# Kernel optimization log

Measured on AMD Instinct MI355X. Metric: run time of the kernel, lower is better.

Reference implementation:

```python
import jax, jax.numpy as jnp
import numpy as np

SIGMAS = (15, 40, 80)  # multi-scale Retinex scales; kernel_size = 2*sigma+1


def _gauss1d(ksize, sigma):
    # kornia.filters.get_gaussian_kernel1d: centered, normalized gaussian
    x = jnp.arange(ksize, dtype=jnp.float32) - (ksize - 1) / 2.0
    g = jnp.exp(-(x * x) / (2.0 * sigma * sigma))
    return g / g.sum()


def _gaussian_blur(img, sigma):
    # img: [B,C,H,W]; kornia gaussian_blur2d: separable depthwise conv,
    # reflect padding, kernel_size = 2*sigma+1
    ksize = int(2 * sigma + 1)
    pad = ksize // 2
    C = img.shape[1]
    k = _gauss1d(ksize, float(sigma))
    xp = jnp.pad(img, ((0, 0), (0, 0), (pad, pad), (pad, pad)), mode='reflect')
    kh = jnp.broadcast_to(k.reshape(1, 1, ksize, 1), (C, 1, ksize, 1))
    kw = jnp.broadcast_to(k.reshape(1, 1, 1, ksize), (C, 1, 1, ksize))
    dn = ('NCHW', 'OIHW', 'NCHW')
    y = jax.lax.conv_general_dilated(xp, kh, (1, 1), 'VALID',
                                     dimension_numbers=dn, feature_group_count=C)
    y = jax.lax.conv_general_dilated(y, kw, (1, 1), 'VALID',
                                     dimension_numbers=dn, feature_group_count=C)
    return y


def setup_inputs() -> dict:
    key = jax.random.key(0)
    B, C, H, W = 8, 3, 1024, 1024
    img = jax.random.uniform(key, (B, C, H, W), dtype=jnp.float32)  # positive, log-safe
    sigmas = jnp.broadcast_to(jnp.array(SIGMAS, dtype=jnp.int32), (B, len(SIGMAS)))
    return {"img": img, "sigmas": sigmas}


def reference(img, sigmas):
    # sigmas determine kernel sizes -> must be static (concrete) values.
    # All batch rows share the same sigma set, so the per-batch loop of the
    # original collapses into batched whole-tensor blurs (identical math).
    sig = np.asarray(sigmas)
    S = sig.shape[1]
    x = img.astype(jnp.float32) + 1e-6
    log_x = jnp.log(x)
    acc = jnp.zeros_like(x)
    for j in range(S):  # small fixed loop over scales (S=3)
        ill = _gaussian_blur(x, int(sig[0, j])) + 1e-6
        acc = acc + (log_x - jnp.log(ill))
    retinex = acc / S
    rmin = retinex.min()
    rmax = retinex.max()
    return (retinex - rmin) / (rmax - rmin) * 255.0
```

## Files before the change

kernel.cpp:

```cpp
#include <hip/hip_runtime.h>
#include <math.h>
#include <string.h>

#define W 1024
#define H 1024
#define HW (1024*1024)
#define NP 24

typedef float  f32x4  __attribute__((ext_vector_type(4)));
typedef short  bf16x8 __attribute__((ext_vector_type(8)));

struct Weights { float w[273]; };

#define P1PIT 328
#define P2P80 328
#define P2P40 264
#define P2P15 200

#define NSLOT 64



__device__ __forceinline__ unsigned fenc(float f) {
  unsigned u = __float_as_uint(f);
  return (u & 0x80000000u) ? ~u : (u | 0x80000000u);
}
__device__ __forceinline__ float fdec(unsigned e) {
  unsigned u = (e & 0x80000000u) ? (e & 0x7fffffffu) : ~e;
  return __uint_as_float(u);
}
__device__ __forceinline__ unsigned bfbits(float f) {
  unsigned u = __float_as_uint(f);
  return (u + 0x7fffu + ((u >> 16) & 1u)) >> 16;
}

__device__ __forceinline__ void minmax_reduce4(float lmn, float lmx, unsigned* mm,
                                               float* red, int slot) {
  #pragma unroll
  for (int off = 32; off > 0; off >>= 1) {
    lmn = fminf(lmn, __shfl_xor(lmn, off));
    lmx = fmaxf(lmx, __shfl_xor(lmx, off));
  }
  const int tid = threadIdx.x;
  const int wid = tid >> 6;
  if ((tid & 63) == 0) { red[wid] = lmn; red[4 + wid] = lmx; }
  __syncthreads();
  if (tid == 0) {
    float mn = fminf(fminf(red[0], red[1]), fminf(red[2], red[3]));
    float mx = fmaxf(fmaxf(red[4], red[5]), fmaxf(red[6], red[7]));
    atomicMin(mm + 2 * slot, fenc(mn));
    atomicMax(mm + 2 * slot + 1, fenc(mx));
  }
}


__global__ void msr_fraginit(Weights wt, ushort* __restrict__ frag, unsigned* __restrict__ mm) {
  const int tid = threadIdx.x;
  if (tid < NSLOT) { mm[2 * tid] = 0xFFFFFFFFu; mm[2 * tid + 1] = 0u; }
  const int pads[3] = {80, 40, 15};
  const int woff[3] = {0, 161, 242};
  const int t0s[3]  = {11, 13, 15};
  for (int e = tid; e < 3 * 6 * 64; e += 256) {
    const int s = e / 384;
    const int rem = e - s * 384;
    const int k = rem >> 6;
    const int lane = rem & 63;
    const int pad = pads[s];
    const int d = pad + (t0s[s] + 2 * k) * 16 - 256;
    ushort* dst = frag + e * 8;
    for (int j = 0; j < 8; ++j) {
      const int kk = ((lane >> 4) << 3) + j;
      const int c  = lane & 15;
      const int idx = d + kk - c;
      float v = (idx >= 0 && idx <= 2 * pad) ? wt.w[woff[s] + idx] : 0.f;
      dst[j] = (ushort)bfbits(v);
    }
  }
}


__global__ void msr_mmred(unsigned* __restrict__ mm) {
  const int tid = threadIdx.x;
  unsigned e = mm[2 * tid];
  unsigned f = mm[2 * tid + 1];
  #pragma unroll
  for (int off = 32; off > 0; off >>= 1) {
    unsigned eo = (unsigned)__shfl_xor((int)e, off);
    unsigned fo = (unsigned)__shfl_xor((int)f, off);
    e = eo < e ? eo : e;
    f = fo > f ? fo : f;
  }
  if (tid == 0) { mm[2 * NSLOT] = e; mm[2 * NSLOT + 1] = f; }
}


template<int NK, int C0, int FB>
__device__ __forceinline__ void h_round(const short* __restrict__ lds,
                                        const bf16x8* __restrict__ fragv,
                                        ushort* __restrict__ pT,
                                        int lane, int rowshort, int x16, int yin) {
  bf16x8 fr[NK];
  #pragma unroll
  for (int k = 0; k < NK; ++k) fr[k] = fragv[(FB + k) * 64 + lane];
  #pragma unroll
  for (int tx = 0; tx < 8; ++tx) {
    f32x4 acc = {0.f, 0.f, 0.f, 0.f};
    #pragma unroll
    for (int k = 0; k < NK; ++k) {
      bf16x8 a = *(const bf16x8*)(lds + rowshort + tx * 16 + C0 + 32 * k);
      acc = __builtin_amdgcn_mfma_f32_16x16x32_bf16(a, fr[k], acc, 0, 0, 0);
    }
    const unsigned lo = bfbits(acc[0]) | (bfbits(acc[1]) << 16);
    const unsigned hi = bfbits(acc[2]) | (bfbits(acc[3]) << 16);
    *(uint2*)(pT + (size_t)(x16 + tx * 16) * 32 + yin) = make_uint2(lo, hi);
  }
}

__global__ __launch_bounds__(128, 3) void msr_hblur3(
    const float* __restrict__ img, ushort* __restrict__ planesT,
    const bf16x8* __restrict__ fragv) {
  __shared__ __align__(16) short lds[32 * P1PIT];
  const int tid = threadIdx.x;
  const int orig = blockIdx.x + (blockIdx.y << 3) + (blockIdx.z << 8);
  const int l = (orig & 7) * 768 + (orig >> 3);
  const int bx = l & 7;
  const int by = (l >> 3) & 31;
  const int bp = l >> 8;
  const int x0 = bx * 128, y0 = by * 32;
  const float* sp = img + (size_t)bp * HW;
  const int row = tid >> 2, c4 = tid & 3;
  const bool interior = (bx >= 1 && bx <= 6);
  #pragma unroll
  for (int it = 0; it < 20; ++it) {
    const int ccpx = 4 * c4 + 16 * it;
    const int gx0 = x0 - 96 + ccpx;
    unsigned lo, hi;
    if (interior || (gx0 >= 0 && gx0 + 4 <= W)) {
      const float4 v = *(const float4*)(sp + (size_t)(y0 + row) * W + gx0);
      lo = bfbits(v.x) | (bfbits(v.y) << 16);
      hi = bfbits(v.z) | (bfbits(v.w) << 16);
    } else {
      unsigned us[4];
      #pragma unroll
      for (int j = 0; j < 4; ++j) {
        int gx = gx0 + j;
        gx = gx < 0 ? -gx : (gx >= W ? 2 * W - 2 - gx : gx);
        us[j] = bfbits(sp[(size_t)(y0 + row) * W + gx]);
      }
      lo = us[0] | (us[1] << 16); hi = us[2] | (us[3] << 16);
    }
    *(uint2*)(lds + row * P1PIT + ccpx) = make_uint2(lo, hi);
  }
  __syncthreads();

  const int lane = tid & 63;
  const int wrow = (tid >> 6) * 16;
  const int q = lane >> 4;
  const int rowshort = (wrow + (lane & 15)) * P1PIT + q * 8;
  const int x16 = x0 + (lane & 15);
  const int yin = wrow + q * 4;
  const size_t sb = (size_t)by * 32768;

  h_round<6, 16, 0>(lds, fragv, planesT + (size_t)(0 * NP + bp) * HW + sb, lane, rowshort, x16, yin);
  h_round<4, 48, 6>(lds, fragv, planesT + (size_t)(1 * NP + bp) * HW + sb, lane, rowshort, x16, yin);
  h_round<2, 80, 12>(lds, fragv, planesT + (size_t)(2 * NP + bp) * HW + sb, lane, rowshort, x16, yin);
}


template<int NCH, int WD>
__device__ __forceinline__ void p2_prefetch(const ushort* __restrict__ pTs, int xrow,
                                            int ystart, int c4, uint4 (&pre)[10]) {
  #pragma unroll
  for (int i = 0; i < NCH; ++i) {
    const int ccpx = 8 * c4 + 32 * i;
    if (ccpx < WD) {
      const int gy = ystart + ccpx;
      if (gy >= 0 && gy + 8 <= H) {
        pre[i] = *(const uint4*)(pTs + (size_t)(gy >> 5) * 32768 + (size_t)xrow * 32 + (gy & 31));
      } else {
        union { ushort u[8]; uint4 v; } t;
        #pragma unroll
        for (int j = 0; j < 8; ++j) {
          int g = gy + j;
          g = g < 0 ? -g : (g >= H ? 2 * H - 2 - g : g);
          t.u[j] = pTs[(size_t)(g >> 5) * 32768 + (size_t)xrow * 32 + (g & 31)];
        }
        pre[i] = t.v;
      }
    }
  }
}

template<int NCH, int WD, int PIT>
__device__ __forceinline__ void p2_wlds(short* __restrict__ lds, int row, int c4,
                                        const uint4 (&pre)[10]) {
  #pragma unroll
  for (int i = 0; i < NCH; ++i) {
    const int ccpx = 8 * c4 + 32 * i;
    if (ccpx < WD) *(uint4*)(lds + row * PIT + ccpx) = pre[i];
  }
}

template<int NK, int PIT, int FB>
__device__ __forceinline__ void p2_convlog(const short* __restrict__ lds,
                                           const bf16x8* __restrict__ fragv,
                                           int lane, int wrow, float* accL) {
  const int rowshort = (wrow + (lane & 15)) * PIT + (lane >> 4) * 8;
  bf16x8 fr[NK];
  #pragma unroll
  for (int k = 0; k < NK; ++k) fr[k] = fragv[(FB + k) * 64 + lane];
  #pragma unroll
  for (int tx = 0; tx < 8; ++tx) {
    f32x4 acc = {0.f, 0.f, 0.f, 0.f};
    #pragma unroll
    for (int k = 0; k < NK; ++k) {
      bf16x8 a = *(const bf16x8*)(lds + rowshort + tx * 16 + 32 * k);
      acc = __builtin_amdgcn_mfma_f32_16x16x32_bf16(a, fr[k], acc, 0, 0, 0);
    }
    #pragma unroll
    for (int r = 0; r < 4; ++r) accL[tx * 4 + r] -= __logf(acc[r] + 2e-6f);
  }
}

__global__ __launch_bounds__(256) __attribute__((amdgpu_waves_per_eu(2, 3)))
void msr_vblur3(
    const ushort* __restrict__ planesT, const float* __restrict__ img,
    float* __restrict__ out, const bf16x8* __restrict__ fragv, unsigned* __restrict__ mm) {
  __shared__ __align__(16) short lds[64 * P2P80];
  __shared__ float red[8];
  const int tid = threadIdx.x;
  const int orig = blockIdx.x + (blockIdx.y << 4) + (blockIdx.z << 7);
  const int l = (orig & 7) * 384 + (orig >> 3);
  const int byt = l & 7;
  const int bxt = (l >> 3) & 15;
  const int bp = l >> 7;
  const int x0 = bxt * 64, y0 = byt * 128;
  const int row = tid >> 2, c4 = tid & 3;
  const int lane = tid & 63;
  const int wrow = (tid >> 6) * 16;
  const int q = lane >> 4;
  const int xb = x0 + wrow + 4 * q;
  const int ycb = y0 + (lane & 15);

  const ushort* pT0 = planesT + (size_t)(0 * NP + bp) * HW;
  const ushort* pT1 = planesT + (size_t)(1 * NP + bp) * HW;
  const ushort* pT2 = planesT + (size_t)(2 * NP + bp) * HW;

  uint4 pre[10];
  p2_prefetch<10, 304>(pT0, x0 + row, y0 - 80, c4, pre);

  float accL[32];
  const float* ip = img + (size_t)bp * HW;
  #pragma unroll
  for (int tx = 0; tx < 8; ++tx) {
    const float4 v = *(const float4*)(ip + (size_t)(ycb + tx * 16) * W + xb);
    accL[tx * 4 + 0] = 3.f * __logf(v.x + 1e-6f);
    accL[tx * 4 + 1] = 3.f * __logf(v.y + 1e-6f);
    accL[tx * 4 + 2] = 3.f * __logf(v.z + 1e-6f);
    accL[tx * 4 + 3] = 3.f * __logf(v.w + 1e-6f);
  }

  p2_wlds<10, 304, P2P80>(lds, row, c4, pre);
  __syncthreads();
  p2_prefetch<8, 240>(pT1, x0 + row, y0 - 48, c4, pre);
  p2_convlog<6, P2P80, 0>(lds, fragv, lane, wrow, accL);
  __syncthreads();
  p2_wlds<8, 240, P2P40>(lds, row, c4, pre);
  __syncthreads();
  p2_prefetch<6, 176>(pT2, x0 + row, y0 - 16, c4, pre);
  p2_convlog<4, P2P40, 6>(lds, fragv, lane, wrow, accL);
  __syncthreads();
  p2_wlds<6, 176, P2P15>(lds, row, c4, pre);
  __syncthreads();
  p2_convlog<2, P2P15, 12>(lds, fragv, lane, wrow, accL);

  float* op = out + (size_t)bp * HW;
  float lmn = 3.4e38f, lmx = -3.4e38f;
  #pragma unroll
  for (int tx = 0; tx < 8; ++tx) {
    #pragma unroll
    for (int r = 0; r < 4; ++r) {
      lmn = fminf(lmn, accL[tx * 4 + r]);
      lmx = fmaxf(lmx, accL[tx * 4 + r]);
    }
    *(float4*)(op + (size_t)(ycb + tx * 16) * W + xb) =
        make_float4(accL[tx * 4 + 0], accL[tx * 4 + 1], accL[tx * 4 + 2], accL[tx * 4 + 3]);
  }
  minmax_reduce4(lmn, lmx, mm, red, orig & (NSLOT - 1));
}


__global__ __launch_bounds__(256) void msr_norm(float* __restrict__ out,
                                                const unsigned* __restrict__ mm) {
  const size_t i = ((size_t)blockIdx.x * 256 + threadIdx.x) * 4;
  const float mn = fdec(mm[2 * NSLOT]);
  const float mx = fdec(mm[2 * NSLOT + 1]);
  const float sc = 255.f / (mx - mn);
  float4 v = *(float4*)(out + i);
  v.x = (v.x - mn) * sc;
  v.y = (v.y - mn) * sc;
  v.z = (v.z - mn) * sc;
  v.w = (v.w - mn) * sc;
  *(float4*)(out + i) = v;
}


static void compute_weights(Weights* wt) {
  memset(wt, 0, sizeof(Weights));
  const int   ntap[3]  = {161, 81, 31};
  const int   off[3]   = {0, 161, 242};
  const float sigma[3] = {80.f, 40.f, 15.f};
  for (int s = 0; s < 3; ++s) {
    const int k = ntap[s];
    float g[161];
    float sum = 0.f;
    for (int i = 0; i < k; ++i) {
      float x = (float)i - (float)(k - 1) * 0.5f;
      g[i] = expf(-(x * x) / (2.f * sigma[s] * sigma[s]));
      sum += g[i];
    }
    const float inv = 1.f / sum;
    for (int i = 0; i < k; ++i) wt->w[off[s] + i] = g[i] * inv;
  }
}


extern "C" void kernel_launch(void* const* d_in, const int* in_sizes, int n_in,
                              void* d_out, int out_size, void* d_ws, size_t ws_size,
                              hipStream_t stream) {
  const float* img = (const float*)d_in[0];
  float* out = (float*)d_out;
  unsigned* mm = (unsigned*)d_ws;
  ushort* frag = (ushort*)((char*)d_ws + 1024);
  ushort* planesT = (ushort*)((char*)d_ws + 32768);

  Weights wt;
  compute_weights(&wt);

  msr_fraginit<<<1, 256, 0, stream>>>(wt, frag, mm);
  msr_hblur3<<<dim3(8, 32, NP), 128, 0, stream>>>(img, planesT, (const bf16x8*)frag);
  msr_vblur3<<<dim3(16, 8, NP), 256, 0, stream>>>(planesT, img, out, (const bf16x8*)frag, mm);
  msr_mmred<<<1, 64, 0, stream>>>(mm);
  msr_norm<<<(unsigned)((size_t)NP * HW / 1024), 256, 0, stream>>>(out, mm);
}
```

Before: 263.4 us.

## Read sigma-15 vertical blur operands directly from global and fold min/max reduction into norm

The sigma-15 vertical pass now loads bf16 MFMA A-fragments straight from the transposed plane in global memory. Reflect-boundary handling is done per element only in edge tiles, so the LDS staging, prefetch and two barriers for that scale are gone. Separately, the single-block min/max reduction kernel is removed: every norm block redoes the 64-slot reduction itself, which saves one launch but repeats a small amount of work per block. The direct global loads may be less coalesced than the LDS path.

```diff
diff --git a/kernel.cpp b/kernel.cpp
--- a/kernel.cpp
+++ b/kernel.cpp
@@ -15,7 +15,6 @@
 #define P1PIT 328
 #define P2P80 328
 #define P2P40 264
-#define P2P15 200
 
 #define NSLOT 64
 
@@ -79,21 +78,6 @@
 }
 
 
-__global__ void msr_mmred(unsigned* __restrict__ mm) {
-  const int tid = threadIdx.x;
-  unsigned e = mm[2 * tid];
-  unsigned f = mm[2 * tid + 1];
-  #pragma unroll
-  for (int off = 32; off > 0; off >>= 1) {
-    unsigned eo = (unsigned)__shfl_xor((int)e, off);
-    unsigned fo = (unsigned)__shfl_xor((int)f, off);
-    e = eo < e ? eo : e;
-    f = fo > f ? fo : f;
-  }
-  if (tid == 0) { mm[2 * NSLOT] = e; mm[2 * NSLOT + 1] = f; }
-}
-
-
 template<int NK, int C0, int FB>
 __device__ __forceinline__ void h_round(const short* __restrict__ lds,
                                         const bf16x8* __restrict__ fragv,
@@ -222,6 +206,40 @@
   }
 }
 
+__device__ __forceinline__ void p2_conv15g(const ushort* __restrict__ pTs,
+                                           const bf16x8* __restrict__ fragv,
+                                           int xa, int ybase, int lane, bool interior,
+                                           float* accL) {
+  bf16x8 fr[2];
+  fr[0] = fragv[12 * 64 + lane];
+  fr[1] = fragv[13 * 64 + lane];
+  const size_t xoff = (size_t)xa << 5;
+  #pragma unroll
+  for (int tx = 0; tx < 8; ++tx) {
+    f32x4 acc = {0.f, 0.f, 0.f, 0.f};
+    #pragma unroll
+    for (int k = 0; k < 2; ++k) {
+      const int y = ybase - 16 + tx * 16 + 32 * k;
+      bf16x8 a;
+      if (interior || (unsigned)y <= (unsigned)(H - 8)) {
+        a = *(const bf16x8*)(pTs + (((size_t)(unsigned)(y >> 5)) << 15) + xoff + (y & 31));
+      } else {
+        union { ushort u[8]; bf16x8 v; } t;
+        #pragma unroll
+        for (int j = 0; j < 8; ++j) {
+          int g = y + j;
+          g = g < 0 ? -g : (g >= H ? 2 * H - 2 - g : g);
+          t.u[j] = pTs[(((size_t)(g >> 5)) << 15) + xoff + (g & 31)];
+        }
+        a = t.v;
+      }
+      acc = __builtin_amdgcn_mfma_f32_16x16x32_bf16(a, fr[k], acc, 0, 0, 0);
+    }
+    #pragma unroll
+    for (int r = 0; r < 4; ++r) accL[tx * 4 + r] -= __logf(acc[r] + 2e-6f);
+  }
+}
+
 __global__ __launch_bounds__(256) __attribute__((amdgpu_waves_per_eu(2, 3)))
 void msr_vblur3(
     const ushort* __restrict__ planesT, const float* __restrict__ img,
@@ -239,8 +257,11 @@
   const int lane = tid & 63;
   const int wrow = (tid >> 6) * 16;
   const int q = lane >> 4;
+  const int xa = x0 + wrow + (lane & 15);
+  const int ybase = y0 + q * 8;
   const int xb = x0 + wrow + 4 * q;
   const int ycb = y0 + (lane & 15);
+  const bool interior = (byt >= 1 && byt <= 6);
 
   const ushort* pT0 = planesT + (size_t)(0 * NP + bp) * HW;
   const ushort* pT1 = planesT + (size_t)(1 * NP + bp) * HW;
@@ -267,12 +288,8 @@
   __syncthreads();
   p2_wlds<8, 240, P2P40>(lds, row, c4, pre);
   __syncthreads();
-  p2_prefetch<6, 176>(pT2, x0 + row, y0 - 16, c4, pre);
   p2_convlog<4, P2P40, 6>(lds, fragv, lane, wrow, accL);
-  __syncthreads();
-  p2_wlds<6, 176, P2P15>(lds, row, c4, pre);
-  __syncthreads();
-  p2_convlog<2, P2P15, 12>(lds, fragv, lane, wrow, accL);
+  p2_conv15g(pT2, fragv, xa, ybase, lane, interior, accL);
 
   float* op = out + (size_t)bp * HW;
   float lmn = 3.4e38f, lmx = -3.4e38f;
@@ -292,10 +309,27 @@
 
 __global__ __launch_bounds__(256) void msr_norm(float* __restrict__ out,
                                                 const unsigned* __restrict__ mm) {
+  __shared__ float smn, ssc;
+  const int tid = threadIdx.x;
+  if (tid < 64) {
+    unsigned e = mm[2 * tid];
+    unsigned f = mm[2 * tid + 1];
+    #pragma unroll
+    for (int off = 32; off > 0; off >>= 1) {
+      unsigned eo = (unsigned)__shfl_xor((int)e, off);
+      unsigned fo = (unsigned)__shfl_xor((int)f, off);
+      e = eo < e ? eo : e;
+      f = fo > f ? fo : f;
+    }
+    if (tid == 0) {
+      const float mn = fdec(e), mx = fdec(f);
+      smn = mn;
+      ssc = 255.f / (mx - mn);
+    }
+  }
+  __syncthreads();
+  const float mn = smn, sc = ssc;
   const size_t i = ((size_t)blockIdx.x * 256 + threadIdx.x) * 4;
-  const float mn = fdec(mm[2 * NSLOT]);
-  const float mx = fdec(mm[2 * NSLOT + 1]);
-  const float sc = 255.f / (mx - mn);
   float4 v = *(float4*)(out + i);
   v.x = (v.x - mn) * sc;
   v.y = (v.y - mn) * sc;
@@ -340,6 +374,5 @@
   msr_fraginit<<<1, 256, 0, stream>>>(wt, frag, mm);
   msr_hblur3<<<dim3(8, 32, NP), 128, 0, stream>>>(img, planesT, (const bf16x8*)frag);
   msr_vblur3<<<dim3(16, 8, NP), 256, 0, stream>>>(planesT, img, out, (const bf16x8*)frag, mm);
-  msr_mmred<<<1, 64, 0, stream>>>(mm);
   msr_norm<<<(unsigned)((size_t)NP * HW / 1024), 256, 0, stream>>>(out, mm);
 }
```

New measurement: 280.6 us. 1.07x slower.

## Store intermediate retinex as bf16 and fold min/max reduction into normalize kernel

Applied to the files above, without the earlier changes.

The vertical blur kernel now writes the unnormalized retinex map as bf16 into a workspace buffer instead of fp32 into the output, which halves that intermediate write and the normalize pass's read. The separate single-block min/max reduction kernel is removed; each normalize block reduces the 64 partial slots itself, saving one launch. In exchange the retinex values lose precision to bf16 before normalization to 0..255, which raises output error, and every normalize block repeats the small reduction.

```diff
diff --git a/kernel.cpp b/kernel.cpp
--- a/kernel.cpp
+++ b/kernel.cpp
@@ -79,21 +79,6 @@
 }
 
 
-__global__ void msr_mmred(unsigned* __restrict__ mm) {
-  const int tid = threadIdx.x;
-  unsigned e = mm[2 * tid];
-  unsigned f = mm[2 * tid + 1];
-  #pragma unroll
-  for (int off = 32; off > 0; off >>= 1) {
-    unsigned eo = (unsigned)__shfl_xor((int)e, off);
-    unsigned fo = (unsigned)__shfl_xor((int)f, off);
-    e = eo < e ? eo : e;
-    f = fo > f ? fo : f;
-  }
-  if (tid == 0) { mm[2 * NSLOT] = e; mm[2 * NSLOT + 1] = f; }
-}
-
-
 template<int NK, int C0, int FB>
 __device__ __forceinline__ void h_round(const short* __restrict__ lds,
                                         const bf16x8* __restrict__ fragv,
@@ -225,7 +210,7 @@
 __global__ __launch_bounds__(256) __attribute__((amdgpu_waves_per_eu(2, 3)))
 void msr_vblur3(
     const ushort* __restrict__ planesT, const float* __restrict__ img,
-    float* __restrict__ out, const bf16x8* __restrict__ fragv, unsigned* __restrict__ mm) {
+    ushort* __restrict__ ret, const bf16x8* __restrict__ fragv, unsigned* __restrict__ mm) {
   __shared__ __align__(16) short lds[64 * P2P80];
   __shared__ float red[8];
   const int tid = threadIdx.x;
@@ -274,7 +259,7 @@
   __syncthreads();
   p2_convlog<2, P2P15, 12>(lds, fragv, lane, wrow, accL);
 
-  float* op = out + (size_t)bp * HW;
+  ushort* rp = ret + (size_t)bp * HW;
   float lmn = 3.4e38f, lmx = -3.4e38f;
   #pragma unroll
   for (int tx = 0; tx < 8; ++tx) {
@@ -283,25 +268,50 @@
       lmn = fminf(lmn, accL[tx * 4 + r]);
       lmx = fmaxf(lmx, accL[tx * 4 + r]);
     }
-    *(float4*)(op + (size_t)(ycb + tx * 16) * W + xb) =
-        make_float4(accL[tx * 4 + 0], accL[tx * 4 + 1], accL[tx * 4 + 2], accL[tx * 4 + 3]);
+    const unsigned lo = bfbits(accL[tx * 4 + 0]) | (bfbits(accL[tx * 4 + 1]) << 16);
+    const unsigned hi = bfbits(accL[tx * 4 + 2]) | (bfbits(accL[tx * 4 + 3]) << 16);
+    *(uint2*)(rp + (size_t)(ycb + tx * 16) * W + xb) = make_uint2(lo, hi);
   }
   minmax_reduce4(lmn, lmx, mm, red, orig & (NSLOT - 1));
 }
 
 
-__global__ __launch_bounds__(256) void msr_norm(float* __restrict__ out,
+__global__ __launch_bounds__(256) void msr_norm(const ushort* __restrict__ ret,
+                                                float* __restrict__ out,
                                                 const unsigned* __restrict__ mm) {
-  const size_t i = ((size_t)blockIdx.x * 256 + threadIdx.x) * 4;
-  const float mn = fdec(mm[2 * NSLOT]);
-  const float mx = fdec(mm[2 * NSLOT + 1]);
-  const float sc = 255.f / (mx - mn);
-  float4 v = *(float4*)(out + i);
-  v.x = (v.x - mn) * sc;
-  v.y = (v.y - mn) * sc;
-  v.z = (v.z - mn) * sc;
-  v.w = (v.w - mn) * sc;
-  *(float4*)(out + i) = v;
+  __shared__ float smn, ssc;
+  const int tid = threadIdx.x;
+  if (tid < 64) {
+    unsigned e = mm[2 * tid];
+    unsigned f = mm[2 * tid + 1];
+    #pragma unroll
+    for (int off = 32; off > 0; off >>= 1) {
+      unsigned eo = (unsigned)__shfl_xor((int)e, off);
+      unsigned fo = (unsigned)__shfl_xor((int)f, off);
+      e = eo < e ? eo : e;
+      f = fo > f ? fo : f;
+    }
+    if (tid == 0) {
+      const float mn = fdec(e), mx = fdec(f);
+      smn = mn;
+      ssc = 255.f / (mx - mn);
+    }
+  }
+  __syncthreads();
+  const float mn = smn, sc = ssc;
+  const size_t i = ((size_t)blockIdx.x * 256 + tid) * 8;
+  const uint4 v = *(const uint4*)(ret + i);
+  float4 o0, o1;
+  o0.x = (__uint_as_float(v.x << 16)          - mn) * sc;
+  o0.y = (__uint_as_float(v.x & 0xFFFF0000u)  - mn) * sc;
+  o0.z = (__uint_as_float(v.y << 16)          - mn) * sc;
+  o0.w = (__uint_as_float(v.y & 0xFFFF0000u)  - mn) * sc;
+  o1.x = (__uint_as_float(v.z << 16)          - mn) * sc;
+  o1.y = (__uint_as_float(v.z & 0xFFFF0000u)  - mn) * sc;
+  o1.z = (__uint_as_float(v.w << 16)          - mn) * sc;
+  o1.w = (__uint_as_float(v.w & 0xFFFF0000u)  - mn) * sc;
+  *(float4*)(out + i) = o0;
+  *(float4*)(out + i + 4) = o1;
 }
 
 
@@ -333,13 +343,13 @@
   unsigned* mm = (unsigned*)d_ws;
   ushort* frag = (ushort*)((char*)d_ws + 1024);
   ushort* planesT = (ushort*)((char*)d_ws + 32768);
+  ushort* ret = (ushort*)((char*)d_ws + 32768 + (size_t)3 * NP * HW * 2);
 
   Weights wt;
   compute_weights(&wt);
 
   msr_fraginit<<<1, 256, 0, stream>>>(wt, frag, mm);
   msr_hblur3<<<dim3(8, 32, NP), 128, 0, stream>>>(img, planesT, (const bf16x8*)frag);
-  msr_vblur3<<<dim3(16, 8, NP), 256, 0, stream>>>(planesT, img, out, (const bf16x8*)frag, mm);
-  msr_mmred<<<1, 64, 0, stream>>>(mm);
-  msr_norm<<<(unsigned)((size_t)NP * HW / 1024), 256, 0, stream>>>(out, mm);
-}
+  msr_vblur3<<<dim3(16, 8, NP), 256, 0, stream>>>(planesT, img, ret, (const bf16x8*)frag, mm);
+  msr_norm<<<(unsigned)((size_t)NP * HW / 2048), 256, 0, stream>>>(ret, out, mm);
+}
```

Measured after the change: 256.4 us. 2.7% less time.
